# Performance work log

Measured on AMD Instinct MI355X. Metric: run time of the kernel, lower is better.

Reference implementation:

```python
import jax, jax.numpy as jnp
import numpy as np
import math

N_HEAD = 16
EPS = 1e-5
GELU_C = math.sqrt(2.0 / math.pi)

def _layernorm(v, w):
    # LN with weight only (bias=None), matching the module's quirky constructor
    mu = jnp.mean(v, axis=-1, keepdims=True)
    var = jnp.mean(jnp.square(v - mu), axis=-1, keepdims=True)
    return (v - mu) * jax.lax.rsqrt(var + EPS) * w

def _new_gelu(x):
    return 0.5 * x * (1.0 + jnp.tanh(GELU_C * (x + 0.044715 * x ** 3)))

def setup_inputs() -> dict:
    key = jax.random.key(0)
    k1, k2, k3, k4 = jax.random.split(key, 4)
    B, T, C = 2, 2048, 2048
    x = jax.random.normal(k1, (B, T, C), dtype=jnp.float32)
    w_qkv = jax.random.normal(k2, (C, 3 * C), dtype=jnp.float32) * 0.02
    w1 = jax.random.normal(k3, (C, 4 * C), dtype=jnp.float32) * 0.02
    w2 = jax.random.normal(k4, (4 * C, C), dtype=jnp.float32) * 0.02
    ln_w = jnp.ones((C,), dtype=jnp.float32)
    return {"x": x, "w_qkv": w_qkv, "w1": w1, "w2": w2, "ln_w": ln_w}

def reference(x, w_qkv, w1, w2, ln_w):
    B, T, C = x.shape
    H = N_HEAD
    D = C // H
    # --- attention branch (pre-LN, shared ln weight) ---
    h = _layernorm(x, ln_w)
    qkv = h @ w_qkv  # [B,T,3C]
    q, k, v = jnp.split(qkv, 3, axis=-1)
    q = q.reshape(B, T, H, D)
    k = k.reshape(B, T, H, D)
    v = v.reshape(B, T, H, D)
    scale = 1.0 / math.sqrt(D)
    att = jnp.einsum('bthd,bshd->bhts', q, k) * scale  # [B,H,T,T]
    causal = jnp.tril(jnp.ones((T, T), dtype=bool))
    att = jnp.where(causal, att, -jnp.inf)
    att = jax.nn.softmax(att, axis=-1)
    attn_out = jnp.einsum('bhts,bshd->bthd', att, v).reshape(B, T, C)
    x = x + attn_out  # note: no output projection in this module
    # --- MLP branch (same ln weight reused) ---
    h2 = _layernorm(x, ln_w)
    mlp = _new_gelu(h2 @ w1) @ w2
    return x + mlp
```

## Files before the change

### kernel.cpp

```cpp
#include <hip/hip_runtime.h>
#include <hip/hip_bf16.h>
#include <math.h>

typedef __bf16 BF16;
typedef __attribute__((ext_vector_type(8))) __bf16 bf16x8;
typedef __attribute__((ext_vector_type(4))) float f32x4;

__device__ __forceinline__ void gld_lds16(const void* g, void* l) {
    __builtin_amdgcn_global_load_lds(
        (__attribute__((address_space(1))) void*)(const void*)g,
        (__attribute__((address_space(3))) void*)l, 16, 0, 0);
}

template <int N> __device__ __forceinline__ void vmwait() {
    if constexpr (N == 0) asm volatile("s_waitcnt vmcnt(0)" ::: "memory");
    else if constexpr (N == 1) asm volatile("s_waitcnt vmcnt(1)" ::: "memory");
    else if constexpr (N == 2) asm volatile("s_waitcnt vmcnt(2)" ::: "memory");
    else if constexpr (N == 3) asm volatile("s_waitcnt vmcnt(3)" ::: "memory");
    else if constexpr (N == 4) asm volatile("s_waitcnt vmcnt(4)" ::: "memory");
    else if constexpr (N == 8) asm volatile("s_waitcnt vmcnt(8)" ::: "memory");
}

__device__ __forceinline__ void barrier_() {
    asm volatile("" ::: "memory");
    __builtin_amdgcn_s_barrier();
    asm volatile("" ::: "memory");
}

__global__ __launch_bounds__(256) void lnorm(const float* __restrict__ x,
                                             const float* __restrict__ w,
                                             BF16* __restrict__ out) {
    const int row = blockIdx.x, tid = threadIdx.x;
    const float* xr = x + (size_t)row * 2048;
    float4 a = *(const float4*)(xr + tid * 8);
    float4 b = *(const float4*)(xr + tid * 8 + 4);
    float s1 = a.x + a.y + a.z + a.w + b.x + b.y + b.z + b.w;
    float s2 = a.x*a.x + a.y*a.y + a.z*a.z + a.w*a.w +
               b.x*b.x + b.y*b.y + b.z*b.z + b.w*b.w;
    #pragma unroll
    for (int off = 32; off; off >>= 1) {
        s1 += __shfl_xor(s1, off);
        s2 += __shfl_xor(s2, off);
    }
    __shared__ float red[8];
    const int l = tid & 63, wv = tid >> 6;
    if (l == 0) { red[wv] = s1; red[4 + wv] = s2; }
    __syncthreads();
    s1 = red[0] + red[1] + red[2] + red[3];
    s2 = red[4] + red[5] + red[6] + red[7];
    const float mean = s1 * (1.0f / 2048.0f);
    const float var  = s2 * (1.0f / 2048.0f) - mean * mean;
    const float rstd = rsqrtf(var + 1e-5f);
    float4 wa = *(const float4*)(w + tid * 8);
    float4 wb = *(const float4*)(w + tid * 8 + 4);
    bf16x8 o;
    o[0] = (BF16)((a.x - mean) * rstd * wa.x);
    o[1] = (BF16)((a.y - mean) * rstd * wa.y);
    o[2] = (BF16)((a.z - mean) * rstd * wa.z);
    o[3] = (BF16)((a.w - mean) * rstd * wa.w);
    o[4] = (BF16)((b.x - mean) * rstd * wb.x);
    o[5] = (BF16)((b.y - mean) * rstd * wb.y);
    o[6] = (BF16)((b.z - mean) * rstd * wb.z);
    o[7] = (BF16)((b.w - mean) * rstd * wb.w);
    *(bf16x8*)(out + (size_t)row * 2048 + tid * 8) = o;
}

__global__ __launch_bounds__(256) void wtrans(const float* __restrict__ W,
                                              BF16* __restrict__ Wt,
                                              int K, int N) {
    __shared__ BF16 tile[32][33];
    const int n0 = blockIdx.x * 32, k0 = blockIdx.y * 32;
    const int tx = threadIdx.x, ty = threadIdx.y;
    #pragma unroll
    for (int i = 0; i < 4; i++)
        tile[ty + 8 * i][tx] = (BF16)W[(size_t)(k0 + ty + 8 * i) * N + n0 + tx];
    __syncthreads();
    #pragma unroll
    for (int i = 0; i < 4; i++)
        Wt[(size_t)(n0 + ty + 8 * i) * K + k0 + tx] = tile[tx][ty + 8 * i];
}

__global__ __launch_bounds__(256) void vtrans(const BF16* __restrict__ qkv,
                                              BF16* __restrict__ vT) {
    __shared__ BF16 tile[32][33];
    const int t0 = blockIdx.x * 32, d0 = blockIdx.y * 32, bh = blockIdx.z;
    const int b = bh >> 4, h = bh & 15;
    const int tx = threadIdx.x, ty = threadIdx.y;
    const BF16* src = qkv + (size_t)b * 2048 * 6144 + 4096 + h * 128;
    #pragma unroll
    for (int i = 0; i < 4; i++)
        tile[ty + 8 * i][tx] = src[(size_t)(t0 + ty + 8 * i) * 6144 + d0 + tx];
    __syncthreads();
    BF16* dst = vT + (size_t)bh * 128 * 2048;
    #pragma unroll
    for (int i = 0; i < 4; i++)
        dst[(size_t)(d0 + ty + 8 * i) * 2048 + t0 + tx] = tile[tx][ty + 8 * i];
}


#define LDA(BI, M_, MH, KK) ({ \
    const int r_ = wm * 64 + (M_) * 16 + c; \
    *(const bf16x8*)(Ab + (BI) * 32768 + (MH) * 16384 + r_ * 128 + \
                     ((((KK) * 4 + g) ^ (r_ & 7)) << 4)); })

#define LDB(BI, N_, KK) ({ \
    const int r_ = wn * (BN / 4) + (N_) * 16 + c; \
    *(const bf16x8*)(Bb + (BI) * BBUF + (KK) * BKU + r_ * 64 + \
                     ((g ^ (r_ & 3)) << 4)); })

#define STA(SI, MH, TS) do { \
    _Pragma("unroll") \
    for (int j_ = 0; j_ < 2; ++j_) { \
        const int r_ = j_ * 64 + (tid >> 3); \
        const int sl_ = (tid & 7) ^ (r_ & 7); \
        gld_lds16(A + (size_t)(m0 + (MH) * 128 + r_) * K + (TS) * 64 + sl_ * 8, \
                  Ab + (SI) * 32768 + (MH) * 16384 + j_ * 8192 + w * 1024); \
    } \
} while (0)

#define STB(SI, KU, TS) do { \
    _Pragma("unroll") \
    for (int j_ = 0; j_ < LBU; ++j_) { \
        const int r_ = j_ * 128 + (tid >> 2); \
        const int sl_ = (tid & 3) ^ (r_ & 3); \
        gld_lds16(Bt + (size_t)(n0 + r_) * K + (TS) * 64 + (KU) * 32 + sl_ * 8, \
                  Bb + (SI) * BBUF + (KU) * BKU + j_ * 8192 + w * 1024); \
    } \
} while (0)

#define MFMA_CL(MH, AF, BF) do { \
    __builtin_amdgcn_s_setprio(1); \
    _Pragma("unroll") \
    for (int m_ = 0; m_ < 4; ++m_) \
      _Pragma("unroll") \
      for (int n_ = 0; n_ < NR; ++n_) \
        acc[(MH) * 4 + m_][n_] = __builtin_amdgcn_mfma_f32_16x16x32_bf16( \
            (AF)[m_], (BF)[n_], acc[(MH) * 4 + m_][n_], 0, 0, 0); \
    __builtin_amdgcn_s_setprio(0); \
} while (0)

#define GBODY(BI, T, ST) do { \
    bf16x8 bfr[NR], af[4]; \
    _Pragma("unroll") for (int n_ = 0; n_ < NR; ++n_) bfr[n_] = LDB(BI, n_, 0); \
    _Pragma("unroll") for (int m_ = 0; m_ < 4; ++m_) af[m_] = LDA(BI, m_, 0, 0); \
    if (ST) STB((BI) ^ 1, 0, (T) + 1); \
    barrier_(); \
    MFMA_CL(0, af, bfr); \
    if (ST) vmwait<2 * LBU>(); else vmwait<0>(); \
    barrier_(); \
    _Pragma("unroll") for (int m_ = 0; m_ < 4; ++m_) af[m_] = LDA(BI, m_, 1, 0); \
    if (ST) STA((BI) ^ 1, 0, (T) + 1); \
    barrier_(); \
    MFMA_CL(1, af, bfr); \
    if (ST) vmwait<LBU + 2>(); \
    barrier_(); \
    _Pragma("unroll") for (int n_ = 0; n_ < NR; ++n_) bfr[n_] = LDB(BI, n_, 1); \
    _Pragma("unroll") for (int m_ = 0; m_ < 4; ++m_) af[m_] = LDA(BI, m_, 0, 1); \
    if (ST) STA((BI) ^ 1, 1, (T) + 1); \
    barrier_(); \
    MFMA_CL(0, af, bfr); \
    barrier_(); \
    _Pragma("unroll") for (int m_ = 0; m_ < 4; ++m_) af[m_] = LDA(BI, m_, 1, 1); \
    if (ST) STB((BI) ^ 1, 1, (T) + 1); \
    barrier_(); \
    MFMA_CL(1, af, bfr); \
    if (ST) vmwait<LBU + 2>(); \
    barrier_(); \
} while (0)

template <int MODE, int BN>
__global__ __launch_bounds__(512) void gemmT(const BF16* __restrict__ A,
                                             const BF16* __restrict__ Bt,
                                             void* __restrict__ out,
                                             const float* __restrict__ resid,
                                             int M, int N, int K) {
    constexpr int NR   = BN / 64;
    constexpr int LBU  = BN / 128;
    constexpr int BKU  = BN * 64;
    constexpr int BBUF = BN * 128;
    (void)M;

    extern __shared__ char smem[];
    char* const Ab = smem;
    char* const Bb = smem + 65536;

    const int tid = threadIdx.x, l = tid & 63, w = tid >> 6;
    const int wm = w >> 2, wn = w & 3;
    const int g = l >> 4, c = l & 15;

    const int NBX = N / BN;
    const int cpx = (int)gridDim.x >> 3;
    const int bid = (int)blockIdx.x;
    const int wg  = (bid & 7) * cpx + (bid >> 3);
    const int m0 = (wg / NBX) * 256, n0 = (wg % NBX) * BN;

    f32x4 acc[8][NR] = {};

    STB(0, 0, 0); STA(0, 0, 0); STA(0, 1, 0); STB(0, 1, 0);
    vmwait<LBU + 2>();
    barrier_();

    const int NT = K >> 6;
    for (int t = 0; t < NT - 2; t += 2) {
        GBODY(0, t, true);
        GBODY(1, t + 1, true);
    }
    GBODY(0, NT - 2, true);
    GBODY(1, NT - 1, false);

    #pragma unroll
    for (int mi = 0; mi < 8; mi++)
      #pragma unroll
      for (int ni = 0; ni < NR; ni++)
        #pragma unroll
        for (int j = 0; j < 4; j++) {
            const int row = m0 + (mi >> 2) * 128 + wm * 64 + (mi & 3) * 16 + g * 4 + j;
            const int col = n0 + wn * (BN / 4) + ni * 16 + c;
            const float v = acc[mi][ni][j];
            const size_t idx = (size_t)row * N + col;
            if (MODE == 0) {
                ((BF16*)out)[idx] = (BF16)v;
            } else if (MODE == 1) {
                const float t2 = v + 0.044715f * v * v * v;
                const float s = 1.0f / (1.0f + __expf(-1.5957691216057308f * t2));
                ((BF16*)out)[idx] = (BF16)(v * s);
            } else {
                ((float*)out)[idx] = resid[idx] + v;
            }
        }
}

__global__ __launch_bounds__(256) void attn(const BF16* __restrict__ qkv,
                                            const BF16* __restrict__ vT,
                                            const float* __restrict__ x,
                                            float* __restrict__ x2) {
    __shared__ BF16 Ks[2][64 * 128];
    __shared__ BF16 Vs[2][128 * 64];
    __shared__ BF16 Ps[4][16 * 72];
    const int tid = threadIdx.x, l = tid & 63, w = tid >> 6;
    const int g = l >> 4, c = l & 15;
    const int bid = (int)blockIdx.x;
    const int wg = (bid & 7) * 64 + (bid >> 3);
    const int pair = wg & 15, bh = wg >> 4;
    const int b = bh >> 4, h = bh & 15;
    const int xr = (c & 7) << 4;

    const BF16* qbase = qkv + (size_t)b * 2048 * 6144 + h * 128;
    const char* kbase = (const char*)(qbase + 2048);
    const char* vbase = (const char*)(vT + (size_t)bh * 128 * 2048);

    auto STAGE = [&](int bb, int k0) {
        #pragma unroll
        for (int s = 0; s < 4; ++s) {
            const int rK = (w * 4 + s) * 4 + (l >> 4);
            const int cK = ((l & 15) * 16) ^ ((rK & 7) << 4);
            gld_lds16(kbase + (size_t)(k0 + rK) * 12288 + cK,
                      &Ks[bb][(w * 4 + s) * 512]);
            const int rV = (w * 4 + s) * 8 + (l >> 3);
            const int cV = ((l & 7) * 16) ^ ((rV & 7) << 4);
            gld_lds16(vbase + (size_t)rV * 4096 + (size_t)k0 * 2 + cV,
                      &Vs[bb][(w * 4 + s) * 512]);
        }
    };

    const float scale = 0.08838834764831845f;

    #pragma unroll 1
    for (int seg = 0; seg < 2; ++seg) {
        const int qb = seg ? 31 - pair : pair;
        const int q0 = qb * 64;

        bf16x8 qf[4];
        {
            const BF16* qrow = qbase + (size_t)(q0 + w * 16 + c) * 6144 + g * 8;
            #pragma unroll
            for (int kc = 0; kc < 4; kc++)
                qf[kc] = *(const bf16x8*)(qrow + kc * 32);
        }
        float m[4]    = {-1e30f, -1e30f, -1e30f, -1e30f};
        float lsum[4] = {0.f, 0.f, 0.f, 0.f};
        f32x4 O[8] = {};

        STAGE(0, 0);
        #pragma unroll 1
        for (int kt = 0; kt <= qb; ++kt) {
            if (kt < qb) { STAGE((kt + 1) & 1, (kt + 1) * 64); vmwait<8>(); }
            else vmwait<0>();
            barrier_();
            const char* KsB = (const char*)Ks[kt & 1];
            const char* VsB = (const char*)Vs[kt & 1];

            f32x4 s4[4] = {};
            #pragma unroll
            for (int ni = 0; ni < 4; ni++)
                #pragma unroll
                for (int kc = 0; kc < 4; kc++) {
                    const bf16x8 kf = *(const bf16x8*)(KsB +
                        (ni * 16 + c) * 256 + ((kc * 64 + g * 16) ^ xr));
                    s4[ni] = __builtin_amdgcn_mfma_f32_16x16x32_bf16(
                        qf[kc], kf, s4[ni], 0, 0, 0);
                }

            const bool maskt = (kt == qb);
            float sv[4][4];
            #pragma unroll
            for (int ni = 0; ni < 4; ni++)
                #pragma unroll
                for (int j = 0; j < 4; j++) {
                    const float v = s4[ni][j] * scale;
                    sv[ni][j] = (!maskt || (ni * 16 + c <= w * 16 + g * 4 + j))
                              ? v : -1e30f;
                }

            float sf[4];
            #pragma unroll
            for (int j = 0; j < 4; j++) {
                float tm = fmaxf(fmaxf(sv[0][j], sv[1][j]),
                                 fmaxf(sv[2][j], sv[3][j]));
                tm = fmaxf(tm, __shfl_xor(tm, 1));
                tm = fmaxf(tm, __shfl_xor(tm, 2));
                tm = fmaxf(tm, __shfl_xor(tm, 4));
                tm = fmaxf(tm, __shfl_xor(tm, 8));
                const float mn = fmaxf(m[j], tm);
                sf[j] = __expf(m[j] - mn);
                m[j] = mn;
            }

            float rs[4] = {0.f, 0.f, 0.f, 0.f};
            #pragma unroll
            for (int ni = 0; ni < 4; ni++)
                #pragma unroll
                for (int j = 0; j < 4; j++) {
                    const float p = __expf(sv[ni][j] - m[j]);
                    rs[j] += p;
                    Ps[w][(g * 4 + j) * 72 + ni * 16 + c] = (BF16)p;
                }
            #pragma unroll
            for (int j = 0; j < 4; j++) {
                float t = rs[j];
                t += __shfl_xor(t, 1);
                t += __shfl_xor(t, 2);
                t += __shfl_xor(t, 4);
                t += __shfl_xor(t, 8);
                lsum[j] = lsum[j] * sf[j] + t;
            }
            #pragma unroll
            for (int dn = 0; dn < 8; dn++)
                #pragma unroll
                for (int j = 0; j < 4; j++) O[dn][j] *= sf[j];

            bf16x8 pa[2];
            #pragma unroll
            for (int ks = 0; ks < 2; ks++)
                pa[ks] = *(const bf16x8*)((const char*)Ps[w] +
                             c * 144 + ks * 64 + g * 16);
            #pragma unroll
            for (int dn = 0; dn < 8; dn++)
                #pragma unroll
                for (int ks = 0; ks < 2; ks++) {
                    const bf16x8 vf = *(const bf16x8*)(VsB +
                        (dn * 16 + c) * 128 + ((ks * 64 + g * 16) ^ xr));
                    O[dn] = __builtin_amdgcn_mfma_f32_16x16x32_bf16(
                        pa[ks], vf, O[dn], 0, 0, 0);
                }
            barrier_();
        }

        float inv[4];
        #pragma unroll
        for (int j = 0; j < 4; j++) inv[j] = 1.0f / lsum[j];
        #pragma unroll
        for (int dn = 0; dn < 8; dn++)
            #pragma unroll
            for (int j = 0; j < 4; j++) {
                const int t   = q0 + w * 16 + g * 4 + j;
                const int col = h * 128 + dn * 16 + c;
                const size_t idx = ((size_t)b * 2048 + t) * 2048 + col;
                x2[idx] = x[idx] + O[dn][j] * inv[j];
            }
    }
}

extern "C" void kernel_launch(void* const* d_in, const int* in_sizes, int n_in,
                              void* d_out, int out_size, void* d_ws, size_t ws_size,
                              hipStream_t stream) {
    const float* x     = (const float*)d_in[0];
    const float* w_qkv = (const float*)d_in[1];
    const float* w1    = (const float*)d_in[2];
    const float* w2    = (const float*)d_in[3];
    const float* ln_w  = (const float*)d_in[4];
    float* out = (float*)d_out;

    char* ws = (char*)d_ws;
    BF16* h_buf = (BF16*)ws;  ws += (size_t)4096 * 2048 * 2;
    BF16* qkvb  = (BF16*)ws;  ws += (size_t)4096 * 6144 * 2;
    BF16* vTb   = (BF16*)ws;  ws += (size_t)32 * 128 * 2048 * 2;
    BF16* wqkvT = (BF16*)ws;  ws += (size_t)6144 * 2048 * 2;
    BF16* w1T   = (BF16*)ws;  ws += (size_t)8192 * 2048 * 2;
    BF16* w2T   = (BF16*)ws;  ws += (size_t)2048 * 8192 * 2;
    BF16* mlp1  = (BF16*)ws;  ws += (size_t)4096 * 8192 * 2;

    hipFuncSetAttribute((const void*)&gemmT<0, 256>,
                        hipFuncAttributeMaxDynamicSharedMemorySize, 131072);
    hipFuncSetAttribute((const void*)&gemmT<1, 256>,
                        hipFuncAttributeMaxDynamicSharedMemorySize, 131072);
    hipFuncSetAttribute((const void*)&gemmT<2, 128>,
                        hipFuncAttributeMaxDynamicSharedMemorySize, 98304);

    lnorm<<<4096, 256, 0, stream>>>(x, ln_w, h_buf);
    wtrans<<<dim3(192, 64), dim3(32, 8), 0, stream>>>(w_qkv, wqkvT, 2048, 6144);
    gemmT<0, 256><<<384, 512, 131072, stream>>>(
        h_buf, wqkvT, qkvb, nullptr, 4096, 6144, 2048);
    vtrans<<<dim3(64, 4, 32), dim3(32, 8), 0, stream>>>(qkvb, vTb);
    attn<<<512, 256, 0, stream>>>(qkvb, vTb, x, out);

    lnorm<<<4096, 256, 0, stream>>>(out, ln_w, h_buf);
    wtrans<<<dim3(256, 64), dim3(32, 8), 0, stream>>>(w1, w1T, 2048, 8192);
    gemmT<1, 256><<<512, 512, 131072, stream>>>(
        h_buf, w1T, mlp1, nullptr, 4096, 8192, 2048);
    wtrans<<<dim3(64, 256), dim3(32, 8), 0, stream>>>(w2, w2T, 8192, 2048);
    gemmT<2, 128><<<256, 512, 98304, stream>>>(
        mlp1, w2T, out, out, 4096, 2048, 8192);
}
```

Baseline: 557.5 us.

## Split A tile into K-halves in LDS and use sched barriers in GEMM

Reorganizes the GEMM's A-operand LDS layout so it is staged in two 32-wide K halves, like B, with a new XOR swizzle on row pairs. This lets each K-half be loaded and consumed in sequence, and it moves the vmcnt waits so the first-half data is waited on earlier. Barriers now use sched_barrier instead of asm memory clobbers, which keeps the compiler from moving instructions across them. The risks are different LDS bank-conflict behaviour from the new swizzle and the loss of the memory clobber ordering.

```diff
diff --git a/kernel.cpp b/kernel.cpp
--- a/kernel.cpp
+++ b/kernel.cpp
@@ -13,18 +13,13 @@
 }
 
 template <int N> __device__ __forceinline__ void vmwait() {
-    if constexpr (N == 0) asm volatile("s_waitcnt vmcnt(0)" ::: "memory");
-    else if constexpr (N == 1) asm volatile("s_waitcnt vmcnt(1)" ::: "memory");
-    else if constexpr (N == 2) asm volatile("s_waitcnt vmcnt(2)" ::: "memory");
-    else if constexpr (N == 3) asm volatile("s_waitcnt vmcnt(3)" ::: "memory");
-    else if constexpr (N == 4) asm volatile("s_waitcnt vmcnt(4)" ::: "memory");
-    else if constexpr (N == 8) asm volatile("s_waitcnt vmcnt(8)" ::: "memory");
-}
-
-__device__ __forceinline__ void barrier_() {
-    asm volatile("" ::: "memory");
+    asm volatile("s_waitcnt vmcnt(%0)" :: "i"(N));
+}
+
+__device__ __forceinline__ void SBAR() {
+    __builtin_amdgcn_sched_barrier(0);
     __builtin_amdgcn_s_barrier();
-    asm volatile("" ::: "memory");
+    __builtin_amdgcn_sched_barrier(0);
 }
 
 __global__ __launch_bounds__(256) void lnorm(const float* __restrict__ x,
@@ -98,74 +93,71 @@
 }
 
 
-#define LDA(BI, M_, MH, KK) ({ \
-    const int r_ = wm * 64 + (M_) * 16 + c; \
-    *(const bf16x8*)(Ab + (BI) * 32768 + (MH) * 16384 + r_ * 128 + \
-                     ((((KK) * 4 + g) ^ (r_ & 7)) << 4)); })
-
-#define LDB(BI, N_, KK) ({ \
-    const int r_ = wn * (BN / 4) + (N_) * 16 + c; \
-    *(const bf16x8*)(Bb + (BI) * BBUF + (KK) * BKU + r_ * 64 + \
-                     ((g ^ (r_ & 3)) << 4)); })
-
-#define STA(SI, MH, TS) do { \
+#define STA(SI, KK, TS) do { \
     _Pragma("unroll") \
     for (int j_ = 0; j_ < 2; ++j_) { \
-        const int r_ = j_ * 64 + (tid >> 3); \
-        const int sl_ = (tid & 7) ^ (r_ & 7); \
-        gld_lds16(A + (size_t)(m0 + (MH) * 128 + r_) * K + (TS) * 64 + sl_ * 8, \
-                  Ab + (SI) * 32768 + (MH) * 16384 + j_ * 8192 + w * 1024); \
+        const int r_ = j_ * 128 + (tid >> 2); \
+        const int sl_ = (tid & 3) ^ ((r_ >> 1) & 3); \
+        gld_lds16(A + (size_t)(m0 + r_) * K + (TS) * 64 + (KK) * 32 + sl_ * 8, \
+                  Ab + (SI) * 32768 + (KK) * 16384 + j_ * 8192 + w * 1024); \
     } \
 } while (0)
 
-#define STB(SI, KU, TS) do { \
+#define STB(SI, KK, TS) do { \
     _Pragma("unroll") \
     for (int j_ = 0; j_ < LBU; ++j_) { \
         const int r_ = j_ * 128 + (tid >> 2); \
-        const int sl_ = (tid & 3) ^ (r_ & 3); \
-        gld_lds16(Bt + (size_t)(n0 + r_) * K + (TS) * 64 + (KU) * 32 + sl_ * 8, \
-                  Bb + (SI) * BBUF + (KU) * BKU + j_ * 8192 + w * 1024); \
+        const int sl_ = (tid & 3) ^ ((r_ >> 1) & 3); \
+        gld_lds16(Bt + (size_t)(n0 + r_) * K + (TS) * 64 + (KK) * 32 + sl_ * 8, \
+                  Bb + (SI) * BBUF + (KK) * (BN * 64) + j_ * 8192 + w * 1024); \
     } \
 } while (0)
 
-#define MFMA_CL(MH, AF, BF) do { \
+#define LDA(BI, MH, M_, KK) \
+    (*(const bf16x8*)(Ab + (BI) * 32768 + (KK) * 16384 + \
+        ((MH) * 128 + wm * 64 + (M_) * 16 + c) * 64 + ((g ^ fa) << 4)))
+
+#define LDB(BI, N_, KK) \
+    (*(const bf16x8*)(Bb + (BI) * BBUF + (KK) * (BN * 64) + \
+        (wn * (BN / 4) + (N_) * 16 + c) * 64 + ((g ^ fa) << 4)))
+
+#define MFMA_CL(MH) do { \
     __builtin_amdgcn_s_setprio(1); \
     _Pragma("unroll") \
     for (int m_ = 0; m_ < 4; ++m_) \
       _Pragma("unroll") \
       for (int n_ = 0; n_ < NR; ++n_) \
         acc[(MH) * 4 + m_][n_] = __builtin_amdgcn_mfma_f32_16x16x32_bf16( \
-            (AF)[m_], (BF)[n_], acc[(MH) * 4 + m_][n_], 0, 0, 0); \
+            af[m_], bfr[n_], acc[(MH) * 4 + m_][n_], 0, 0, 0); \
     __builtin_amdgcn_s_setprio(0); \
 } while (0)
 
 #define GBODY(BI, T, ST) do { \
-    bf16x8 bfr[NR], af[4]; \
+    bf16x8 af[4], bfr[NR]; \
     _Pragma("unroll") for (int n_ = 0; n_ < NR; ++n_) bfr[n_] = LDB(BI, n_, 0); \
-    _Pragma("unroll") for (int m_ = 0; m_ < 4; ++m_) af[m_] = LDA(BI, m_, 0, 0); \
+    _Pragma("unroll") for (int m_ = 0; m_ < 4; ++m_) af[m_] = LDA(BI, 0, m_, 0); \
     if (ST) STB((BI) ^ 1, 0, (T) + 1); \
-    barrier_(); \
-    MFMA_CL(0, af, bfr); \
-    if (ST) vmwait<2 * LBU>(); else vmwait<0>(); \
-    barrier_(); \
-    _Pragma("unroll") for (int m_ = 0; m_ < 4; ++m_) af[m_] = LDA(BI, m_, 1, 0); \
+    SBAR(); \
+    MFMA_CL(0); \
+    SBAR(); \
+    _Pragma("unroll") for (int m_ = 0; m_ < 4; ++m_) af[m_] = LDA(BI, 1, m_, 0); \
     if (ST) STA((BI) ^ 1, 0, (T) + 1); \
-    barrier_(); \
-    MFMA_CL(1, af, bfr); \
+    SBAR(); \
+    MFMA_CL(1); \
+    if (ST) vmwait<LBU + 2>(); else vmwait<0>(); \
+    SBAR(); \
+    _Pragma("unroll") for (int n_ = 0; n_ < NR; ++n_) bfr[n_] = LDB(BI, n_, 1); \
+    _Pragma("unroll") for (int m_ = 0; m_ < 4; ++m_) af[m_] = LDA(BI, 0, m_, 1); \
+    if (ST) STB((BI) ^ 1, 1, (T) + 1); \
+    SBAR(); \
+    MFMA_CL(0); \
+    SBAR(); \
+    _Pragma("unroll") for (int m_ = 0; m_ < 4; ++m_) af[m_] = LDA(BI, 1, m_, 1); \
+    if (ST) STA((BI) ^ 1, 1, (T) + 1); \
+    SBAR(); \
+    MFMA_CL(1); \
     if (ST) vmwait<LBU + 2>(); \
-    barrier_(); \
-    _Pragma("unroll") for (int n_ = 0; n_ < NR; ++n_) bfr[n_] = LDB(BI, n_, 1); \
-    _Pragma("unroll") for (int m_ = 0; m_ < 4; ++m_) af[m_] = LDA(BI, m_, 0, 1); \
-    if (ST) STA((BI) ^ 1, 1, (T) + 1); \
-    barrier_(); \
-    MFMA_CL(0, af, bfr); \
-    barrier_(); \
-    _Pragma("unroll") for (int m_ = 0; m_ < 4; ++m_) af[m_] = LDA(BI, m_, 1, 1); \
-    if (ST) STB((BI) ^ 1, 1, (T) + 1); \
-    barrier_(); \
-    MFMA_CL(1, af, bfr); \
-    if (ST) vmwait<LBU + 2>(); \
-    barrier_(); \
+    SBAR(); \
 } while (0)
 
 template <int MODE, int BN>
@@ -176,7 +168,6 @@
                                              int M, int N, int K) {
     constexpr int NR   = BN / 64;
     constexpr int LBU  = BN / 128;
-    constexpr int BKU  = BN * 64;
     constexpr int BBUF = BN * 128;
     (void)M;
 
@@ -187,6 +178,7 @@
     const int tid = threadIdx.x, l = tid & 63, w = tid >> 6;
     const int wm = w >> 2, wn = w & 3;
     const int g = l >> 4, c = l & 15;
+    const int fa = (c >> 1) & 3;
 
     const int NBX = N / BN;
     const int cpx = (int)gridDim.x >> 3;
@@ -196,9 +188,9 @@
 
     f32x4 acc[8][NR] = {};
 
-    STB(0, 0, 0); STA(0, 0, 0); STA(0, 1, 0); STB(0, 1, 0);
+    STB(0, 0, 0); STA(0, 0, 0); STB(0, 1, 0); STA(0, 1, 0);
     vmwait<LBU + 2>();
-    barrier_();
+    SBAR();
 
     const int NT = K >> 6;
     for (int t = 0; t < NT - 2; t += 2) {
@@ -286,7 +278,7 @@
         for (int kt = 0; kt <= qb; ++kt) {
             if (kt < qb) { STAGE((kt + 1) & 1, (kt + 1) * 64); vmwait<8>(); }
             else vmwait<0>();
-            barrier_();
+            SBAR();
             const char* KsB = (const char*)Ks[kt & 1];
             const char* VsB = (const char*)Vs[kt & 1];
 
@@ -363,7 +355,7 @@
                     O[dn] = __builtin_amdgcn_mfma_f32_16x16x32_bf16(
                         pa[ks], vf, O[dn], 0, 0, 0);
                 }
-            barrier_();
+            SBAR();
         }
 
         float inv[4];
```

Measured after the change: 560.2 us, median of 2. About the same (+0.5%).
